# Kernel tuning notes

Measured on AMD Instinct MI355X. Metric: run time of the kernel, lower is better.

## Reference

```python
import jax, jax.numpy as jnp
import numpy as np

N = 500_000        # atoms
P = 16_000_000     # neighbor pairs (half list)
NS = 4             # species types
CUTOFF = 2.5
BOX = 20.0         # cubic box edge length


def setup_inputs() -> dict:
    key = jax.random.key(0)
    k = jax.random.split(key, 6)
    positions = jax.random.uniform(k[0], (N, 3), dtype=jnp.float32) * BOX
    cell = jnp.eye(3, dtype=jnp.float32) * BOX
    pair_i = jax.random.randint(k[1], (P,), 0, N, dtype=jnp.int32)
    # guarantee j != i so r2 > 0 even when shift == 0
    offs = jax.random.randint(k[2], (P,), 1, N, dtype=jnp.int32)
    pair_j = (pair_i + offs) % N
    shifts = jax.random.randint(k[3], (P, 3), 0, 3, dtype=jnp.int32)
    species = jax.random.randint(k[4], (N,), 0, NS, dtype=jnp.int32)
    # per-species-pair LJ parameter tables (symmetric), mirroring the
    # dict {(a,b): (sigma, epsilon)} precomputation in __init__
    sig = 0.8 + 0.1 * jnp.arange(NS, dtype=jnp.float32)
    eps = 0.5 + 0.1 * jnp.arange(NS, dtype=jnp.float32)
    sigma_tab = 0.5 * (sig[:, None] + sig[None, :])
    eps_tab = jnp.sqrt(eps[:, None] * eps[None, :])
    sr = sigma_tab / CUTOFF
    shift_tab = 4.0 * eps_tab * (sr ** 12 - sr ** 6)
    return dict(positions=positions, cell=cell, sigma_tab=sigma_tab,
                eps_tab=eps_tab, shift_tab=shift_tab, species=species,
                pair_i=pair_i, pair_j=pair_j, shifts=shifts)


def reference(positions, cell, sigma_tab, eps_tab, shift_tab,
              species, pair_i, pair_j, shifts):
    # gather species-pair params (vectorized dict lookup)
    si = species[pair_i]
    sj = species[pair_j]
    sigma = sigma_tab[si, sj]        # [P]
    epsilon = eps_tab[si, sj]        # [P]
    shift_e = shift_tab[si, sj]      # [P]
    # displacement with periodic cell shift: r_j - r_i + S @ cell
    d = positions[pair_j] - positions[pair_i] + shifts.astype(positions.dtype) @ cell  # [P,3]
    r2 = jnp.sum(d * d, axis=-1)     # [P]
    r6 = r2 * r2 * r2
    sigma3 = sigma * sigma * sigma
    sigma6 = sigma3 * sigma3
    sr6 = sigma6 / r6
    sr12 = sr6 * sr6
    e = 4.0 * epsilon * (sr12 - sr6) - shift_e   # [P]
    # per-atom energy: half to each endpoint (per_atom=True path)
    energy = jnp.zeros(positions.shape[0], dtype=positions.dtype)
    energy = energy.at[pair_i].add(0.5 * e).at[pair_j].add(0.5 * e)
    return energy
```

## Files before the change

### kernel.cpp

```cpp
#include <hip/hip_runtime.h>


#define BUCKET_SHIFT 11
#define BUCKET_SIZE  2048

__global__ void lj_cursor_init_kernel(int* __restrict__ cursor, int nb, int cap) {
    int i = blockIdx.x * blockDim.x + threadIdx.x;
    if (i < nb) cursor[i] = i * cap;
}

__global__ void lj_zero_kernel(float* __restrict__ out, long n) {
    long i = (long)blockIdx.x * blockDim.x + threadIdx.x;
    if (i < n) out[i] = 0.0f;
}

__global__ void lj_pack_kernel(const float* __restrict__ pos,
                               const int* __restrict__ species,
                               float4* __restrict__ packed, int n) {
    int i = blockIdx.x * blockDim.x + threadIdx.x;
    if (i < n) {
        float4 p;
        p.x = pos[3 * i];
        p.y = pos[3 * i + 1];
        p.z = pos[3 * i + 2];
        p.w = __int_as_float(species[i]);
        packed[i] = p;
    }
}

__device__ __forceinline__ unsigned int lj_encode(float he) {
    unsigned int u = __float_as_uint(he);
    return (u + 0x400u) & 0xFFFFF800u;
}

__global__ __launch_bounds__(256) void lj_passA_kernel(
    const float4* __restrict__ packed,
    const float* __restrict__ cell,
    const float* __restrict__ sigma_tab,
    const float* __restrict__ eps_tab,
    const float* __restrict__ shift_tab,
    const int* __restrict__ pair_i,
    const int* __restrict__ pair_j,
    const int* __restrict__ shifts,
    unsigned int* __restrict__ record_buf,
    int* __restrict__ cursor,
    int cap, int nb, int P)
{
    __shared__ float s_sig6[16];
    __shared__ float s_eps4[16];
    __shared__ float s_shift[16];
    __shared__ float s_cell[9];
    __shared__ int hist[256];
    __shared__ int basev[256];
    int t = threadIdx.x;
    if (t < 16) {
        float s = sigma_tab[t];
        float s3 = s * s * s;
        s_sig6[t] = s3 * s3;
        s_eps4[t] = 4.0f * eps_tab[t];
        s_shift[t] = shift_tab[t];
    }
    if (t < 9) s_cell[t] = cell[t];
    hist[t] = 0;
    __syncthreads();

    float c00 = s_cell[0], c01 = s_cell[1], c02 = s_cell[2];
    float c10 = s_cell[3], c11 = s_cell[4], c12 = s_cell[5];
    float c20 = s_cell[6], c21 = s_cell[7], c22 = s_cell[8];

    long base = (long)(blockIdx.x * (long)blockDim.x + t) * 4;

    int   ai[4], aj[4];
    float hev[4];
    int   sloti[4], slotj[4];
    bool  valid[4];

    if (base + 3 < P) {
        int4 pi4 = *(const int4*)(pair_i + base);
        int4 pj4 = *(const int4*)(pair_j + base);
        int4 sA = *(const int4*)(shifts + base * 3);
        int4 sB = *(const int4*)(shifts + base * 3 + 4);
        int4 sC = *(const int4*)(shifts + base * 3 + 8);
        int pis[4] = {pi4.x, pi4.y, pi4.z, pi4.w};
        int pjs[4] = {pj4.x, pj4.y, pj4.z, pj4.w};
        int shv[12] = {sA.x, sA.y, sA.z, sA.w, sB.x, sB.y, sB.z, sB.w,
                       sC.x, sC.y, sC.z, sC.w};
#pragma unroll
        for (int k = 0; k < 4; ++k) {
            int i = pis[k], j = pjs[k];
            float fx = (float)shv[3 * k], fy = (float)shv[3 * k + 1], fz = (float)shv[3 * k + 2];
            float4 gi = packed[i];
            float4 gj = packed[j];
            float dx = gj.x - gi.x + fx * c00 + fy * c10 + fz * c20;
            float dy = gj.y - gi.y + fx * c01 + fy * c11 + fz * c21;
            float dz = gj.z - gi.z + fx * c02 + fy * c12 + fz * c22;
            float r2 = dx * dx + dy * dy + dz * dz;
            float r6 = r2 * r2 * r2;
            int idx = __float_as_int(gi.w) * 4 + __float_as_int(gj.w);
            float sr6 = s_sig6[idx] / r6;
            float sr12 = sr6 * sr6;
            hev[k] = 0.5f * (s_eps4[idx] * (sr12 - sr6) - s_shift[idx]);
            ai[k] = i; aj[k] = j; valid[k] = true;
        }
    } else {
#pragma unroll
        for (int k = 0; k < 4; ++k) {
            long p = base + k;
            valid[k] = (p < P);
            ai[k] = 0; aj[k] = 0; hev[k] = 0.0f;
            if (valid[k]) {
                int i = pair_i[p], j = pair_j[p];
                float fx = (float)shifts[3 * p], fy = (float)shifts[3 * p + 1], fz = (float)shifts[3 * p + 2];
                float4 gi = packed[i];
                float4 gj = packed[j];
                float dx = gj.x - gi.x + fx * c00 + fy * c10 + fz * c20;
                float dy = gj.y - gi.y + fx * c01 + fy * c11 + fz * c21;
                float dz = gj.z - gi.z + fx * c02 + fy * c12 + fz * c22;
                float r2 = dx * dx + dy * dy + dz * dz;
                float r6 = r2 * r2 * r2;
                int idx = __float_as_int(gi.w) * 4 + __float_as_int(gj.w);
                float sr6 = s_sig6[idx] / r6;
                float sr12 = sr6 * sr6;
                hev[k] = 0.5f * (s_eps4[idx] * (sr12 - sr6) - s_shift[idx]);
                ai[k] = i; aj[k] = j;
            }
        }
    }

#pragma unroll
    for (int k = 0; k < 4; ++k) {
        if (valid[k]) {
            sloti[k] = atomicAdd(&hist[ai[k] >> BUCKET_SHIFT], 1);
            slotj[k] = atomicAdd(&hist[aj[k] >> BUCKET_SHIFT], 1);
        } else {
            sloti[k] = 0; slotj[k] = 0;
        }
    }
    __syncthreads();

    if (t < nb) {
        int h = hist[t];
        basev[t] = (h > 0) ? atomicAdd(&cursor[t], h) : 0;
    }
    __syncthreads();

#pragma unroll
    for (int k = 0; k < 4; ++k) {
        if (valid[k]) {
            unsigned int u = lj_encode(hev[k]);
            int bi = ai[k] >> BUCKET_SHIFT;
            int wi = basev[bi] + sloti[k];
            if (wi < (bi + 1) * cap)
                record_buf[wi] = u | (unsigned int)(ai[k] & (BUCKET_SIZE - 1));
            int bj = aj[k] >> BUCKET_SHIFT;
            int wj = basev[bj] + slotj[k];
            if (wj < (bj + 1) * cap)
                record_buf[wj] = u | (unsigned int)(aj[k] & (BUCKET_SIZE - 1));
        }
    }
}

__global__ __launch_bounds__(256) void lj_passB_kernel(
    const unsigned int* __restrict__ record_buf,
    const int* __restrict__ cursor,
    float* __restrict__ energy,
    int cap, int N)
{
    __shared__ float e[BUCKET_SIZE];
    int b = blockIdx.x;
    int t = threadIdx.x;
#pragma unroll
    for (int k = 0; k < 8; ++k) e[t + 256 * k] = 0.0f;
    __syncthreads();

    int begin = b * cap;
    int count = cursor[b] - begin;
    if (count > cap) count = cap;

    int nfull = count >> 3;
    for (int g = t; g < nfull; g += 256) {
        const unsigned int* rp = record_buf + begin + g * 8;
        int4 a = *(const int4*)(rp);
        int4 c = *(const int4*)(rp + 4);
        unsigned int w0 = (unsigned int)a.x, w1 = (unsigned int)a.y;
        unsigned int w2 = (unsigned int)a.z, w3 = (unsigned int)a.w;
        unsigned int w4 = (unsigned int)c.x, w5 = (unsigned int)c.y;
        unsigned int w6 = (unsigned int)c.z, w7 = (unsigned int)c.w;
        atomicAdd(&e[w0 & 2047u], __uint_as_float(w0 & 0xFFFFF800u));
        atomicAdd(&e[w1 & 2047u], __uint_as_float(w1 & 0xFFFFF800u));
        atomicAdd(&e[w2 & 2047u], __uint_as_float(w2 & 0xFFFFF800u));
        atomicAdd(&e[w3 & 2047u], __uint_as_float(w3 & 0xFFFFF800u));
        atomicAdd(&e[w4 & 2047u], __uint_as_float(w4 & 0xFFFFF800u));
        atomicAdd(&e[w5 & 2047u], __uint_as_float(w5 & 0xFFFFF800u));
        atomicAdd(&e[w6 & 2047u], __uint_as_float(w6 & 0xFFFFF800u));
        atomicAdd(&e[w7 & 2047u], __uint_as_float(w7 & 0xFFFFF800u));
    }
    int tail0 = nfull * 8;
    int r = tail0 + t;
    if (r < count) {
        unsigned int w = record_buf[begin + r];
        atomicAdd(&e[w & 2047u], __uint_as_float(w & 0xFFFFF800u));
    }
    __syncthreads();

    int a0 = b * BUCKET_SIZE;
#pragma unroll
    for (int k = 0; k < 8; ++k) {
        int a = a0 + t + 256 * k;
        if (a < N) energy[a] = e[t + 256 * k];
    }
}

__device__ __forceinline__ void lj_one_pair_packed(
    int i, int j, float fx, float fy, float fz,
    const float4* __restrict__ packed,
    const float* s_sig6, const float* s_eps4, const float* s_shift,
    float c00, float c01, float c02,
    float c10, float c11, float c12,
    float c20, float c21, float c22,
    float* __restrict__ energy)
{
    float4 gi = packed[i];
    float4 gj = packed[j];
    float dx = gj.x - gi.x + fx * c00 + fy * c10 + fz * c20;
    float dy = gj.y - gi.y + fx * c01 + fy * c11 + fz * c21;
    float dz = gj.z - gi.z + fx * c02 + fy * c12 + fz * c22;
    float r2 = dx * dx + dy * dy + dz * dz;
    float r6 = r2 * r2 * r2;
    int idx = __float_as_int(gi.w) * 4 + __float_as_int(gj.w);
    float sr6 = s_sig6[idx] / r6;
    float sr12 = sr6 * sr6;
    float he = 0.5f * (s_eps4[idx] * (sr12 - sr6) - s_shift[idx]);
    atomicAdd(energy + i, he);
    atomicAdd(energy + j, he);
}

__global__ __launch_bounds__(256) void lj_pairs_packed_kernel(
    const float4* __restrict__ packed,
    const float* __restrict__ cell,
    const float* __restrict__ sigma_tab,
    const float* __restrict__ eps_tab,
    const float* __restrict__ shift_tab,
    const int* __restrict__ pair_i,
    const int* __restrict__ pair_j,
    const int* __restrict__ shifts,
    float* __restrict__ energy,
    int P)
{
    __shared__ float s_sig6[16];
    __shared__ float s_eps4[16];
    __shared__ float s_shift[16];
    __shared__ float s_cell[9];
    int t = threadIdx.x;
    if (t < 16) {
        float s = sigma_tab[t];
        float s3 = s * s * s;
        s_sig6[t] = s3 * s3;
        s_eps4[t] = 4.0f * eps_tab[t];
        s_shift[t] = shift_tab[t];
    }
    if (t < 9) s_cell[t] = cell[t];
    __syncthreads();

    float c00 = s_cell[0], c01 = s_cell[1], c02 = s_cell[2];
    float c10 = s_cell[3], c11 = s_cell[4], c12 = s_cell[5];
    float c20 = s_cell[6], c21 = s_cell[7], c22 = s_cell[8];

    long base = (long)(blockIdx.x * (long)blockDim.x + t) * 4;
    if (base + 3 < P) {
        int4 pi4 = *(const int4*)(pair_i + base);
        int4 pj4 = *(const int4*)(pair_j + base);
        int4 sA = *(const int4*)(shifts + base * 3);
        int4 sB = *(const int4*)(shifts + base * 3 + 4);
        int4 sC = *(const int4*)(shifts + base * 3 + 8);
        int pis[4] = {pi4.x, pi4.y, pi4.z, pi4.w};
        int pjs[4] = {pj4.x, pj4.y, pj4.z, pj4.w};
        int shv[12] = {sA.x, sA.y, sA.z, sA.w, sB.x, sB.y, sB.z, sB.w,
                       sC.x, sC.y, sC.z, sC.w};
#pragma unroll
        for (int k = 0; k < 4; ++k) {
            lj_one_pair_packed(pis[k], pjs[k],
                        (float)shv[3 * k], (float)shv[3 * k + 1], (float)shv[3 * k + 2],
                        packed, s_sig6, s_eps4, s_shift,
                        c00, c01, c02, c10, c11, c12, c20, c21, c22, energy);
        }
    } else {
        for (long p = base; p < P; ++p) {
            lj_one_pair_packed(pair_i[p], pair_j[p],
                        (float)shifts[3 * p], (float)shifts[3 * p + 1], (float)shifts[3 * p + 2],
                        packed, s_sig6, s_eps4, s_shift,
                        c00, c01, c02, c10, c11, c12, c20, c21, c22, energy);
        }
    }
}

__device__ __forceinline__ void lj_one_pair(
    int i, int j, float fx, float fy, float fz,
    const float* __restrict__ pos,
    const int* __restrict__ species,
    const float* s_sig6, const float* s_eps4, const float* s_shift,
    float c00, float c01, float c02,
    float c10, float c11, float c12,
    float c20, float c21, float c22,
    float* __restrict__ energy)
{
    float dx = pos[3 * j]     - pos[3 * i]     + fx * c00 + fy * c10 + fz * c20;
    float dy = pos[3 * j + 1] - pos[3 * i + 1] + fx * c01 + fy * c11 + fz * c21;
    float dz = pos[3 * j + 2] - pos[3 * i + 2] + fx * c02 + fy * c12 + fz * c22;
    float r2 = dx * dx + dy * dy + dz * dz;
    float r6 = r2 * r2 * r2;
    int idx = species[i] * 4 + species[j];
    float sr6 = s_sig6[idx] / r6;
    float sr12 = sr6 * sr6;
    float he = 0.5f * (s_eps4[idx] * (sr12 - sr6) - s_shift[idx]);
    atomicAdd(energy + i, he);
    atomicAdd(energy + j, he);
}

__global__ __launch_bounds__(256) void lj_pairs_kernel(
    const float* __restrict__ pos,
    const float* __restrict__ cell,
    const float* __restrict__ sigma_tab,
    const float* __restrict__ eps_tab,
    const float* __restrict__ shift_tab,
    const int* __restrict__ species,
    const int* __restrict__ pair_i,
    const int* __restrict__ pair_j,
    const int* __restrict__ shifts,
    float* __restrict__ energy,
    int P)
{
    __shared__ float s_sig6[16];
    __shared__ float s_eps4[16];
    __shared__ float s_shift[16];
    __shared__ float s_cell[9];
    int t = threadIdx.x;
    if (t < 16) {
        float s = sigma_tab[t];
        float s3 = s * s * s;
        s_sig6[t] = s3 * s3;
        s_eps4[t] = 4.0f * eps_tab[t];
        s_shift[t] = shift_tab[t];
    }
    if (t < 9) s_cell[t] = cell[t];
    __syncthreads();

    float c00 = s_cell[0], c01 = s_cell[1], c02 = s_cell[2];
    float c10 = s_cell[3], c11 = s_cell[4], c12 = s_cell[5];
    float c20 = s_cell[6], c21 = s_cell[7], c22 = s_cell[8];

    long base = (long)(blockIdx.x * (long)blockDim.x + t) * 4;
    if (base + 3 < P) {
        int4 pi4 = *(const int4*)(pair_i + base);
        int4 pj4 = *(const int4*)(pair_j + base);
        int4 sA = *(const int4*)(shifts + base * 3);
        int4 sB = *(const int4*)(shifts + base * 3 + 4);
        int4 sC = *(const int4*)(shifts + base * 3 + 8);
        int pis[4] = {pi4.x, pi4.y, pi4.z, pi4.w};
        int pjs[4] = {pj4.x, pj4.y, pj4.z, pj4.w};
        int shv[12] = {sA.x, sA.y, sA.z, sA.w, sB.x, sB.y, sB.z, sB.w,
                       sC.x, sC.y, sC.z, sC.w};
#pragma unroll
        for (int k = 0; k < 4; ++k) {
            lj_one_pair(pis[k], pjs[k],
                        (float)shv[3 * k], (float)shv[3 * k + 1], (float)shv[3 * k + 2],
                        pos, species, s_sig6, s_eps4, s_shift,
                        c00, c01, c02, c10, c11, c12, c20, c21, c22, energy);
        }
    } else {
        for (long p = base; p < P; ++p) {
            lj_one_pair(pair_i[p], pair_j[p],
                        (float)shifts[3 * p], (float)shifts[3 * p + 1], (float)shifts[3 * p + 2],
                        pos, species, s_sig6, s_eps4, s_shift,
                        c00, c01, c02, c10, c11, c12, c20, c21, c22, energy);
        }
    }
}

extern "C" void kernel_launch(void* const* d_in, const int* in_sizes, int n_in,
                              void* d_out, int out_size, void* d_ws, size_t ws_size,
                              hipStream_t stream) {
    const float* positions = (const float*)d_in[0];
    const float* cell      = (const float*)d_in[1];
    const float* sigma_tab = (const float*)d_in[2];
    const float* eps_tab   = (const float*)d_in[3];
    const float* shift_tab = (const float*)d_in[4];
    const int*   species   = (const int*)d_in[5];
    const int*   pair_i    = (const int*)d_in[6];
    const int*   pair_j    = (const int*)d_in[7];
    const int*   shifts    = (const int*)d_in[8];
    float* energy = (float*)d_out;

    const int N = out_size;
    const int P = in_sizes[6];

    const int threads = 256;
    const int ablocks = (N + threads - 1) / threads;
    const int pblocks4 = (int)((((long)P + 3) / 4 + threads - 1) / threads);

    const int nb = (N + BUCKET_SIZE - 1) / BUCKET_SIZE;
    long avg = (2L * P) / (nb > 0 ? nb : 1);
    long capl = (avg + avg / 50 + 512 + 1023) & ~1023L;
    const int cap = (int)capl;
    const size_t rec_bytes  = (size_t)nb * (size_t)cap * 4u;
    const size_t pack_bytes = (size_t)N * 16u;
    const size_t cur_bytes  = (size_t)nb * 4u;
    const size_t need_bucket = rec_bytes + pack_bytes + cur_bytes;
    const size_t need_pack   = pack_bytes;

    const bool has_ws = (d_ws != nullptr);
    const bool sane = (nb > 0) && (nb <= 256) && ((long)nb * cap < 2000000000L);
    const bool use_bucket = has_ws && sane && (ws_size >= need_bucket);
    const bool use_pack   = has_ws && !use_bucket && (ws_size >= need_pack);

    if (use_bucket) {
        unsigned int* record_buf = (unsigned int*)d_ws;
        float4* packed = (float4*)((char*)d_ws + rec_bytes);
        int* cursor = (int*)((char*)d_ws + rec_bytes + pack_bytes);

        lj_cursor_init_kernel<<<1, 256, 0, stream>>>(cursor, nb, cap);
        lj_pack_kernel<<<ablocks, threads, 0, stream>>>(positions, species, packed, N);
        lj_passA_kernel<<<pblocks4, threads, 0, stream>>>(
            packed, cell, sigma_tab, eps_tab, shift_tab,
            pair_i, pair_j, shifts, record_buf, cursor, cap, nb, P);
        lj_passB_kernel<<<nb, threads, 0, stream>>>(record_buf, cursor, energy, cap, N);
    } else if (use_pack) {
        float4* packed = (float4*)d_ws;
        lj_zero_kernel<<<ablocks, threads, 0, stream>>>(energy, N);
        lj_pack_kernel<<<ablocks, threads, 0, stream>>>(positions, species, packed, N);
        lj_pairs_packed_kernel<<<pblocks4, threads, 0, stream>>>(
            packed, cell, sigma_tab, eps_tab, shift_tab,
            pair_i, pair_j, shifts, energy, P);
    } else {
        lj_zero_kernel<<<ablocks, threads, 0, stream>>>(energy, N);
        lj_pairs_kernel<<<pblocks4, threads, 0, stream>>>(
            positions, cell, sigma_tab, eps_tab, shift_tab, species,
            pair_i, pair_j, shifts, energy, P);
    }
}
```

Before: 897.9 us.

## Split each pass-B bucket across eight blocks with partial sums and reduce

Pass B previously ran one block per bucket, so only about 245 blocks worked through roughly 130K records each, which underfills the GPU's compute units. Each bucket is now split into eight slices handled by separate blocks, and each block writes its shared-memory histogram to a partial buffer. A new reduce kernel sums the eight partials per atom. This raises parallelism at the cost of extra workspace, an extra kernel launch, and about 16 MB of partial-buffer traffic.

```diff
diff --git a/kernel.cpp b/kernel.cpp
--- a/kernel.cpp
+++ b/kernel.cpp
@@ -3,6 +3,7 @@
 
 #define BUCKET_SHIFT 11
 #define BUCKET_SIZE  2048
+#define SLICES       8
 
 __global__ void lj_cursor_init_kernel(int* __restrict__ cursor, int nb, int cap) {
     int i = blockIdx.x * blockDim.x + threadIdx.x;
@@ -163,11 +164,13 @@
 __global__ __launch_bounds__(256) void lj_passB_kernel(
     const unsigned int* __restrict__ record_buf,
     const int* __restrict__ cursor,
-    float* __restrict__ energy,
-    int cap, int N)
+    float* __restrict__ partial,
+    int cap)
 {
     __shared__ float e[BUCKET_SIZE];
-    int b = blockIdx.x;
+    int blk = blockIdx.x;
+    int b = blk >> 3;
+    int s = blk & (SLICES - 1);
     int t = threadIdx.x;
 #pragma unroll
     for (int k = 0; k < 8; ++k) e[t + 256 * k] = 0.0f;
@@ -177,37 +180,55 @@
     int count = cursor[b] - begin;
     if (count > cap) count = cap;
 
-    int nfull = count >> 3;
-    for (int g = t; g < nfull; g += 256) {
-        const unsigned int* rp = record_buf + begin + g * 8;
-        int4 a = *(const int4*)(rp);
-        int4 c = *(const int4*)(rp + 4);
-        unsigned int w0 = (unsigned int)a.x, w1 = (unsigned int)a.y;
-        unsigned int w2 = (unsigned int)a.z, w3 = (unsigned int)a.w;
-        unsigned int w4 = (unsigned int)c.x, w5 = (unsigned int)c.y;
-        unsigned int w6 = (unsigned int)c.z, w7 = (unsigned int)c.w;
-        atomicAdd(&e[w0 & 2047u], __uint_as_float(w0 & 0xFFFFF800u));
-        atomicAdd(&e[w1 & 2047u], __uint_as_float(w1 & 0xFFFFF800u));
-        atomicAdd(&e[w2 & 2047u], __uint_as_float(w2 & 0xFFFFF800u));
-        atomicAdd(&e[w3 & 2047u], __uint_as_float(w3 & 0xFFFFF800u));
-        atomicAdd(&e[w4 & 2047u], __uint_as_float(w4 & 0xFFFFF800u));
-        atomicAdd(&e[w5 & 2047u], __uint_as_float(w5 & 0xFFFFF800u));
-        atomicAdd(&e[w6 & 2047u], __uint_as_float(w6 & 0xFFFFF800u));
-        atomicAdd(&e[w7 & 2047u], __uint_as_float(w7 & 0xFFFFF800u));
-    }
-    int tail0 = nfull * 8;
-    int r = tail0 + t;
-    if (r < count) {
-        unsigned int w = record_buf[begin + r];
-        atomicAdd(&e[w & 2047u], __uint_as_float(w & 0xFFFFF800u));
-    }
-    __syncthreads();
-
-    int a0 = b * BUCKET_SIZE;
-#pragma unroll
-    for (int k = 0; k < 8; ++k) {
-        int a = a0 + t + 256 * k;
-        if (a < N) energy[a] = e[t + 256 * k];
+    int ngroups = (count + 7) >> 3;
+    int gps = (ngroups + SLICES - 1) / SLICES;
+    int g0 = s * gps;
+    int g1 = g0 + gps;
+    if (g1 > ngroups) g1 = ngroups;
+
+    for (int g = g0 + t; g < g1; g += 256) {
+        int r0 = g * 8;
+        const unsigned int* rp = record_buf + begin + r0;
+        if (r0 + 8 <= count) {
+            int4 a = *(const int4*)(rp);
+            int4 c = *(const int4*)(rp + 4);
+            unsigned int w0 = (unsigned int)a.x, w1 = (unsigned int)a.y;
+            unsigned int w2 = (unsigned int)a.z, w3 = (unsigned int)a.w;
+            unsigned int w4 = (unsigned int)c.x, w5 = (unsigned int)c.y;
+            unsigned int w6 = (unsigned int)c.z, w7 = (unsigned int)c.w;
+            atomicAdd(&e[w0 & 2047u], __uint_as_float(w0 & 0xFFFFF800u));
+            atomicAdd(&e[w1 & 2047u], __uint_as_float(w1 & 0xFFFFF800u));
+            atomicAdd(&e[w2 & 2047u], __uint_as_float(w2 & 0xFFFFF800u));
+            atomicAdd(&e[w3 & 2047u], __uint_as_float(w3 & 0xFFFFF800u));
+            atomicAdd(&e[w4 & 2047u], __uint_as_float(w4 & 0xFFFFF800u));
+            atomicAdd(&e[w5 & 2047u], __uint_as_float(w5 & 0xFFFFF800u));
+            atomicAdd(&e[w6 & 2047u], __uint_as_float(w6 & 0xFFFFF800u));
+            atomicAdd(&e[w7 & 2047u], __uint_as_float(w7 & 0xFFFFF800u));
+        } else {
+            for (int r = r0; r < count; ++r) {
+                unsigned int w = record_buf[begin + r];
+                atomicAdd(&e[w & 2047u], __uint_as_float(w & 0xFFFFF800u));
+            }
+        }
+    }
+    __syncthreads();
+
+    float* pb = partial + (long)blk * BUCKET_SIZE;
+#pragma unroll
+    for (int k = 0; k < 8; ++k) pb[t + 256 * k] = e[t + 256 * k];
+}
+
+__global__ void lj_reduce_kernel(const float* __restrict__ partial,
+                                 float* __restrict__ energy, int N) {
+    int i = blockIdx.x * blockDim.x + threadIdx.x;
+    if (i < N) {
+        int b = i >> BUCKET_SHIFT;
+        int l = i & (BUCKET_SIZE - 1);
+        const float* pb = partial + ((long)b * SLICES) * BUCKET_SIZE + l;
+        float s = 0.0f;
+#pragma unroll
+        for (int k = 0; k < SLICES; ++k) s += pb[(long)k * BUCKET_SIZE];
+        energy[i] = s;
     }
 }
 
@@ -405,7 +426,8 @@
     const size_t rec_bytes  = (size_t)nb * (size_t)cap * 4u;
     const size_t pack_bytes = (size_t)N * 16u;
     const size_t cur_bytes  = (size_t)nb * 4u;
-    const size_t need_bucket = rec_bytes + pack_bytes + cur_bytes;
+    const size_t part_bytes = (size_t)nb * SLICES * BUCKET_SIZE * 4u;
+    const size_t need_bucket = rec_bytes + pack_bytes + cur_bytes + part_bytes;
     const size_t need_pack   = pack_bytes;
 
     const bool has_ws = (d_ws != nullptr);
@@ -417,13 +439,15 @@
         unsigned int* record_buf = (unsigned int*)d_ws;
         float4* packed = (float4*)((char*)d_ws + rec_bytes);
         int* cursor = (int*)((char*)d_ws + rec_bytes + pack_bytes);
+        float* partial = (float*)((char*)d_ws + rec_bytes + pack_bytes + cur_bytes);
 
         lj_cursor_init_kernel<<<1, 256, 0, stream>>>(cursor, nb, cap);
         lj_pack_kernel<<<ablocks, threads, 0, stream>>>(positions, species, packed, N);
         lj_passA_kernel<<<pblocks4, threads, 0, stream>>>(
             packed, cell, sigma_tab, eps_tab, shift_tab,
             pair_i, pair_j, shifts, record_buf, cursor, cap, nb, P);
-        lj_passB_kernel<<<nb, threads, 0, stream>>>(record_buf, cursor, energy, cap, N);
+        lj_passB_kernel<<<nb * SLICES, threads, 0, stream>>>(record_buf, cursor, partial, cap);
+        lj_reduce_kernel<<<ablocks, threads, 0, stream>>>(partial, energy, N);
     } else if (use_pack) {
         float4* packed = (float4*)d_ws;
         lj_zero_kernel<<<ablocks, threads, 0, stream>>>(energy, N);
```

Measured after the change: 902.0 us. About the same (+0.5%).
